# Performance work log

Measured on AMD Instinct MI355X. Metric: run time of the kernel, lower is better.

## Reference

```python
import jax, jax.numpy as jnp
import numpy as np

S, B, D, H, DH = 512, 32, 256, 8, 32  # seq, batch, in_dim, heads, dim_head
LN_EPS = 1e-5


def setup_inputs() -> dict:
    key = jax.random.key(0)
    k1, k2, k3 = jax.random.split(key, 3)
    x = jax.random.normal(k1, (S, B, D), jnp.float32)
    slow_W = jax.random.normal(k2, (H * (5 * DH + 2), D), jnp.float32) * 0.02
    out_W = jax.random.normal(k3, (D, H * DH), jnp.float32) * 0.02
    ln_g = jnp.ones((D,), jnp.float32)
    ln_b = jnp.zeros((D,), jnp.float32)
    return {"x": x, "slow_W": slow_W, "out_W": out_W, "ln_g": ln_g, "ln_b": ln_b}


def elu_p1(x):
    return jax.nn.elu(x) + 1.0


def sum_norm(x):
    return x / jnp.sum(x, axis=-1, keepdims=True)


def layer_norm(x, g, b):
    mu = jnp.mean(x, axis=-1, keepdims=True)
    var = jnp.mean(jnp.square(x - mu), axis=-1, keepdims=True)
    return (x - mu) * jax.lax.rsqrt(var + LN_EPS) * g + b


def _fast_rnn_forward(x, slow_W, out_W, ln_g, ln_b):
    slen, bsz, _ = x.shape
    o = layer_norm(x, ln_g, ln_b)
    qkv = jnp.einsum('sbd,ed->sbe', o, slow_W)  # [S,B,H*(5*DH+2)]
    qkv = qkv.reshape(slen, bsz, H, 5 * DH + 2)
    q, k, v, rk, rv, beta, rbeta = jnp.split(
        qkv, [DH, 2 * DH, 3 * DH, 4 * DH, 5 * DH, 5 * DH + 1], axis=-1)
    beta = jax.nn.sigmoid(beta)      # [S,B,H,1]
    rbeta = jax.nn.sigmoid(rbeta)    # [S,B,H,1]
    q = sum_norm(elu_p1(q))
    k = sum_norm(elu_p1(k))
    rk = jax.nn.softmax(rk, axis=-1)

    # ---- feed-forward fast weights with delta rule (fast_weight_delta) ----
    def ff_step(W, inp):
        qt, kt, vt, bt = inp                      # [B,H,DH], bt [B,H,1]
        v_old = jnp.einsum('bhij,bhj->bhi', W, kt)
        W = W + ((bt * (vt - v_old))[..., :, None] * kt[..., None, :])
        z = jnp.einsum('bhij,bhj->bhi', W, qt)
        return W, z

    W0 = jnp.zeros((bsz, H, DH, DH), x.dtype)
    _, z = jax.lax.scan(ff_step, W0, (q, k, v, beta))  # z: [S,B,H,DH]

    # ---- recurrent fast weights (fast_rnn_v2): query = softmax(prev state) ----
    def rec_step(carry, inp):
        R, h = carry
        zt, kt, vt, bt = inp
        q_rec = jax.nn.softmax(h, axis=-1)         # query from previous state
        v_old = jnp.einsum('bhij,bhj->bhi', R, kt)
        R = R + ((bt * (vt - v_old))[..., :, None] * kt[..., None, :])
        h = zt + jnp.einsum('bhij,bhj->bhi', R, q_rec)
        return (R, h), h

    R0 = jnp.zeros((bsz, H, DH, DH), x.dtype)
    h0 = jnp.zeros((bsz, H, DH), x.dtype)
    _, hs = jax.lax.scan(rec_step, (R0, h0), (z, rk, rv, rbeta))  # [S,B,H,DH]

    out = hs.reshape(slen, bsz, H * DH)
    out = jnp.einsum('sbe,de->sbd', out, out_W)
    return x + out  # dropout is identity in eval


def reference(x, slow_W, out_W, ln_g, ln_b):
    return _fast_rnn_forward(x, slow_W, out_W, ln_g, ln_b)
```

## Files before the change

kernel.cpp:

```cpp
#include <hip/hip_runtime.h>
#include <hip/hip_bf16.h>
#include <math.h>

#define S_   512
#define B_   32
#define D_   256
#define H_   8
#define DH_  32
#define E_   (H_*(5*DH_+2))
#define SB_  (S_*B_)
#define LN_EPSF 1e-5f

#define ROWP_ 164
#define NPAD_ 1344

typedef short  bf16x8 __attribute__((ext_vector_type(8)));
typedef float  f32x4  __attribute__((ext_vector_type(4)));
typedef float  f32x2  __attribute__((ext_vector_type(2)));

__device__ __forceinline__ float wave_sum64(float v){
  #pragma unroll
  for (int m = 32; m >= 1; m >>= 1) v += __shfl_xor(v, m, 64);
  return v;
}
__device__ __forceinline__ float gsum32(float v){
  #pragma unroll
  for (int m = 16; m >= 1; m >>= 1) v += __shfl_xor(v, m, 32);
  return v;
}
__device__ __forceinline__ float gmax32(float v){
  #pragma unroll
  for (int m = 16; m >= 1; m >>= 1) v = fmaxf(v, __shfl_xor(v, m, 32));
  return v;
}

#if __has_builtin(__builtin_amdgcn_permlane32_swap)
typedef int v2i_ __attribute__((ext_vector_type(2)));
__device__ __forceinline__ float xhalf_sum(float x){
  v2i_ r = __builtin_amdgcn_permlane32_swap(__float_as_int(x), __float_as_int(x), false, false);
  return __int_as_float(r.x) + __int_as_float(r.y);
}
#else
__device__ __forceinline__ float xhalf_sum(float x){
  return x + __shfl_xor(x, 32, 64);
}
#endif

#define GL4(dst, sb, vo, IMM) \
  asm volatile("global_load_dwordx4 %0, %1, %2 offset:" IMM \
               : "=&v"(dst) : "v"(vo), "s"(sb))
#define GL2(dst, sb, vo, IMM) \
  asm volatile("global_load_dwordx2 %0, %1, %2 offset:" IMM \
               : "=&v"(dst) : "v"(vo), "s"(sb))
#define GL1(dst, sb, vo, IMM) \
  asm volatile("global_load_dword %0, %1, %2 offset:" IMM \
               : "=&v"(dst) : "v"(vo), "s"(sb))

__global__ __launch_bounds__(256) void ln_kernel(const float* __restrict__ x,
                                                 const float* __restrict__ g,
                                                 const float* __restrict__ b,
                                                 __hip_bfloat16* __restrict__ o){
  __shared__ float sbuf[4];
  const int row = blockIdx.x, tid = threadIdx.x;
  const float v = x[(size_t)row*D_ + tid];
  float s = wave_sum64(v);
  if ((tid & 63) == 0) sbuf[tid >> 6] = s;
  __syncthreads();
  const float mu = (sbuf[0]+sbuf[1]+sbuf[2]+sbuf[3]) * (1.f/D_);
  __syncthreads();
  const float d = v - mu;
  float s2 = wave_sum64(d*d);
  if ((tid & 63) == 0) sbuf[tid >> 6] = s2;
  __syncthreads();
  const float var = (sbuf[0]+sbuf[1]+sbuf[2]+sbuf[3]) * (1.f/D_);
  const float rstd = rsqrtf(var + LN_EPSF);
  o[(size_t)row*D_ + tid] = __float2bfloat16(d*rstd*g[tid] + b[tid]);
}

__global__ __launch_bounds__(256) void cvt_w(const float* __restrict__ W1,
                                             const float* __restrict__ W2,
                                             __hip_bfloat16* __restrict__ o1,
                                             __hip_bfloat16* __restrict__ o2){
  const int r = blockIdx.x, c = threadIdx.x;
  if (r < NPAD_){
    const float v = (r < E_) ? W1[(size_t)r*D_ + c] : 0.f;
    o1[(size_t)r*D_ + c] = __float2bfloat16(v);
  } else {
    const int r2 = r - NPAD_;
    o2[(size_t)r2*D_ + c] = __float2bfloat16(W2[(size_t)r2*D_ + c]);
  }
}

__global__ __launch_bounds__(256) void gemm1_mfma(const __hip_bfloat16* __restrict__ A,
                                                  const __hip_bfloat16* __restrict__ Bw,
                                                  float* __restrict__ qkvT){
  const int tid = threadIdx.x;
  const int w = tid >> 6, l = tid & 63;
  const int lr = l & 15, lk = (l >> 4) << 3;
  const int m0 = blockIdx.y*64 + (w>>1)*32;
  const int n0 = blockIdx.x*64 + (w&1)*32;

  const __hip_bfloat16* Ap = A  + (size_t)(m0+lr)*D_ + lk;
  const __hip_bfloat16* Bp = Bw + (size_t)(n0+lr)*D_ + lk;

  f32x4 acc00={0,0,0,0}, acc01={0,0,0,0}, acc10={0,0,0,0}, acc11={0,0,0,0};
  #pragma unroll
  for (int ks = 0; ks < 8; ++ks){
    const bf16x8 a0 = *(const bf16x8*)(Ap + ks*32);
    const bf16x8 a1 = *(const bf16x8*)(Ap + 16*D_ + ks*32);
    const bf16x8 b0 = *(const bf16x8*)(Bp + ks*32);
    const bf16x8 b1 = *(const bf16x8*)(Bp + 16*D_ + ks*32);
    acc00 = __builtin_amdgcn_mfma_f32_16x16x32_bf16(a0, b0, acc00, 0,0,0);
    acc01 = __builtin_amdgcn_mfma_f32_16x16x32_bf16(a0, b1, acc01, 0,0,0);
    acc10 = __builtin_amdgcn_mfma_f32_16x16x32_bf16(a1, b0, acc10, 0,0,0);
    acc11 = __builtin_amdgcn_mfma_f32_16x16x32_bf16(a1, b1, acc11, 0,0,0);
  }

  const int mrow = (l>>4)<<2;
  #pragma unroll
  for (int i=0;i<2;i++){
    #pragma unroll
    for (int j=0;j<2;j++){
      const f32x4 av = (i==0) ? (j==0?acc00:acc01) : (j==0?acc10:acc11);
      const int n = n0 + j*16 + lr;
      if (n < E_){
        const unsigned head = (unsigned)n / 162u;
        const unsigned jj   = (unsigned)n - head*162u;
        #pragma unroll
        for (int reg=0;reg<4;reg++){
          const int m = m0 + i*16 + mrow + reg;
          const int s = m >> 5, bq = m & 31;
          qkvT[((size_t)(bq*8u+head)*S_ + s)*ROWP_ + jj] = av[reg];
        }
      }
    }
  }
}

__global__ __launch_bounds__(256) void gemm2_mfma(const __hip_bfloat16* __restrict__ A,
                                                  const __hip_bfloat16* __restrict__ Bw,
                                                  const float* __restrict__ X,
                                                  float* __restrict__ C){
  const int tid = threadIdx.x;
  const int w = tid >> 6, l = tid & 63;
  const int lr = l & 15, lk = (l >> 4) << 3;
  const int m0 = blockIdx.y*64 + (w>>1)*32;
  const int n0 = blockIdx.x*64 + (w&1)*32;

  const __hip_bfloat16* Ap = A  + (size_t)(m0+lr)*D_ + lk;
  const __hip_bfloat16* Bp = Bw + (size_t)(n0+lr)*D_ + lk;

  f32x4 acc00={0,0,0,0}, acc01={0,0,0,0}, acc10={0,0,0,0}, acc11={0,0,0,0};
  #pragma unroll
  for (int ks = 0; ks < 8; ++ks){
    const bf16x8 a0 = *(const bf16x8*)(Ap + ks*32);
    const bf16x8 a1 = *(const bf16x8*)(Ap + 16*D_ + ks*32);
    const bf16x8 b0 = *(const bf16x8*)(Bp + ks*32);
    const bf16x8 b1 = *(const bf16x8*)(Bp + 16*D_ + ks*32);
    acc00 = __builtin_amdgcn_mfma_f32_16x16x32_bf16(a0, b0, acc00, 0,0,0);
    acc01 = __builtin_amdgcn_mfma_f32_16x16x32_bf16(a0, b1, acc01, 0,0,0);
    acc10 = __builtin_amdgcn_mfma_f32_16x16x32_bf16(a1, b0, acc10, 0,0,0);
    acc11 = __builtin_amdgcn_mfma_f32_16x16x32_bf16(a1, b1, acc11, 0,0,0);
  }

  const int mrow = (l>>4)<<2;
  #pragma unroll
  for (int i=0;i<2;i++){
    #pragma unroll
    for (int j=0;j<2;j++){
      const f32x4 av = (i==0) ? (j==0?acc00:acc01) : (j==0?acc10:acc11);
      const int n = n0 + j*16 + lr;
      #pragma unroll
      for (int reg=0;reg<4;reg++){
        const size_t m = (size_t)(m0 + i*16 + mrow + reg);
        C[m*D_ + n] = av[reg] + X[m*D_ + n];
      }
    }
  }
}

__global__ __launch_bounds__(256) void act2_kernel(float* __restrict__ qkvT){
  const int row = blockIdx.x*8 + (threadIdx.x >> 5);
  const int i = threadIdx.x & 31;
  float* base = qkvT + (size_t)row*ROWP_;
  float qv  = base[i];
  float kv  = base[DH_ + i];
  float rkv = base[3*DH_ + i];
  qv = qv > 0.f ? qv + 1.f : __expf(qv);
  kv = kv > 0.f ? kv + 1.f : __expf(kv);
  const float qs = gsum32(qv);
  const float ks = gsum32(kv);
  const float rm = gmax32(rkv);
  const float re = __expf(rkv - rm);
  const float rs = gsum32(re);
  base[i]         = qv / qs;
  base[DH_ + i]   = kv / ks;
  base[3*DH_ + i] = re / rs;
  if (i < 2){
    const float bv = base[5*DH_ + i];
    base[5*DH_ + i] = 1.f/(1.f + __expf(-bv));
  }
}

#define SCAN_ISSUE(P, sbp)                                                    \
  { const float* sb_ = (sbp);                                                 \
    GL4(P##q0,  sb_, voP, "0");   GL4(P##q1,  sb_, voP, "16");                \
    GL4(P##q2,  sb_, voP, "32");  GL4(P##q3,  sb_, voP, "48");                \
    GL4(P##k0,  sb_, voP, "128"); GL4(P##k1,  sb_, voP, "144");               \
    GL4(P##k2,  sb_, voP, "160"); GL4(P##k3,  sb_, voP, "176");               \
    GL4(P##rk0, sb_, voP, "384"); GL4(P##rk1, sb_, voP, "400");               \
    GL4(P##rk2, sb_, voP, "416"); GL4(P##rk3, sb_, voP, "432");               \
    GL1(P##v,   sb_, voR, "256"); GL1(P##rv,  sb_, voR, "512");               \
    GL2(P##bb,  sb_, voZ, "640"); }

#define SCAN_BODY(P, tt)                                                      \
  {                                                                           \
             \
    const float e_ = __expf(h);                                               \
    ebuf[r] = e_;                                                             \
    f32x4 ev0 = *(const f32x4*)&ebuf[p16+0];                                  \
    f32x4 ev1 = *(const f32x4*)&ebuf[p16+4];                                  \
    f32x4 ev2 = *(const f32x4*)&ebuf[p16+8];                                  \
    f32x4 ev3 = *(const f32x4*)&ebuf[p16+12];                                 \
                                    \
    if ((tt) >= S_-2) { asm volatile("s_waitcnt vmcnt(0)" ::: "memory"); }    \
    else              { asm volatile("s_waitcnt vmcnt(16)" ::: "memory"); }   \
    __builtin_amdgcn_sched_barrier(0);                                        \
    float q_[16], k_[16], rk_[16];                                            \
    *(f32x4*)&q_[0]=P##q0;  *(f32x4*)&q_[4]=P##q1;                            \
    *(f32x4*)&q_[8]=P##q2;  *(f32x4*)&q_[12]=P##q3;                           \
    *(f32x4*)&k_[0]=P##k0;  *(f32x4*)&k_[4]=P##k1;                            \
    *(f32x4*)&k_[8]=P##k2;  *(f32x4*)&k_[12]=P##k3;                           \
    *(f32x4*)&rk_[0]=P##rk0; *(f32x4*)&rk_[4]=P##rk1;                         \
    *(f32x4*)&rk_[8]=P##rk2; *(f32x4*)&rk_[12]=P##rk3;                        \
    const float vv = P##v, rvv = P##rv;                                       \
    const float beta = P##bb.x, rbeta = P##bb.y;                              \
                                                      \
    float a0=0.f,a1=0.f,a2=0.f,a3=0.f;                                        \
    _Pragma("unroll")                                                         \
    for (int c4=0;c4<16;c4+=4){                                               \
      a0=fmaf(W[c4+0],k_[c4+0],a0); a1=fmaf(W[c4+1],k_[c4+1],a1);             \
      a2=fmaf(W[c4+2],k_[c4+2],a2); a3=fmaf(W[c4+3],k_[c4+3],a3);             \
    }                                                                         \
    const float dot1f = xhalf_sum((a0+a1)+(a2+a3));                           \
    const float coeff = beta*(vv - dot1f);                                    \
    float b0=0.f,b1=0.f,b2=0.f,b3=0.f;                                        \
    _Pragma("unroll")                                                         \
    for (int c4=0;c4<16;c4+=4){                                               \
      W[c4+0]=fmaf(coeff,k_[c4+0],W[c4+0]); b0=fmaf(W[c4+0],q_[c4+0],b0);     \
      W[c4+1]=fmaf(coeff,k_[c4+1],W[c4+1]); b1=fmaf(W[c4+1],q_[c4+1],b1);     \
      W[c4+2]=fmaf(coeff,k_[c4+2],W[c4+2]); b2=fmaf(W[c4+2],q_[c4+2],b2);     \
      W[c4+3]=fmaf(coeff,k_[c4+3],W[c4+3]); b3=fmaf(W[c4+3],q_[c4+3],b3);     \
    }                                                                         \
    const float z_ = xhalf_sum((b0+b1)+(b2+b3));                              \
                            \
    float c0=0.f,c1=0.f,c2=0.f,c3=0.f;                                        \
    _Pragma("unroll")                                                         \
    for (int c4=0;c4<16;c4+=4){                                               \
      c0=fmaf(R[c4+0],rk_[c4+0],c0); c1=fmaf(R[c4+1],rk_[c4+1],c1);           \
      c2=fmaf(R[c4+2],rk_[c4+2],c2); c3=fmaf(R[c4+3],rk_[c4+3],c3);           \
    }                                                                         \
    const float dot1r = xhalf_sum((c0+c1)+(c2+c3));                           \
    const float coefr = rbeta*(rvv - dot1r);                                  \
    _Pragma("unroll")                                                         \
    for (int c4=0;c4<16;c4+=4){                                               \
      R[c4+0]=fmaf(coefr,rk_[c4+0],R[c4+0]); R[c4+1]=fmaf(coefr,rk_[c4+1],R[c4+1]); \
      R[c4+2]=fmaf(coefr,rk_[c4+2],R[c4+2]); R[c4+3]=fmaf(coefr,rk_[c4+3],R[c4+3]); \
    }                                                                         \
      \
    float evv[16];                                                            \
    *(f32x4*)&evv[0]=ev0; *(f32x4*)&evv[4]=ev1;                               \
    *(f32x4*)&evv[8]=ev2; *(f32x4*)&evv[12]=ev3;                              \
    float t0=(evv[0]+evv[1])+(evv[2]+evv[3]),   t1=(evv[4]+evv[5])+(evv[6]+evv[7]); \
    float t2=(evv[8]+evv[9])+(evv[10]+evv[11]), t3=(evv[12]+evv[13])+(evv[14]+evv[15]); \
    const float Ss = xhalf_sum((t0+t1)+(t2+t3));                              \
    float d0=0.f,d1=0.f,d2=0.f,d3=0.f;                                        \
    _Pragma("unroll")                                                         \
    for (int c4=0;c4<16;c4+=4){                                               \
      d0=fmaf(R[c4+0],evv[c4+0],d0); d1=fmaf(R[c4+1],evv[c4+1],d1);           \
      d2=fmaf(R[c4+2],evv[c4+2],d2); d3=fmaf(R[c4+3],evv[c4+3],d3);           \
    }                                                                         \
    const float dot2 = xhalf_sum((d0+d1)+(d2+d3));                            \
    h = fmaf(dot2, __builtin_amdgcn_rcpf(Ss), z_);                            \
    hsb[(size_t)(tt)*(B_*D_) + hoff] = __float2bfloat16(h);                   \
                                       \
    if ((tt)+2 < S_) SCAN_ISSUE(P, gbase + (size_t)((tt)+2)*ROWP_);           \
  }

__global__ __launch_bounds__(64,1) void scan_fused2(const float* __restrict__ qkvT,
                                                    __hip_bfloat16* __restrict__ hsb){
  const int pair = blockIdx.x;
  const int lane = threadIdx.x;
  const int r = lane & 31, p = lane >> 5;
  const int p16 = p*16;
  const int b = pair >> 3, hh = pair & 7;
  const float* gbase = qkvT + (size_t)pair*S_*ROWP_;
  const size_t hoff = (size_t)b*D_ + hh*DH_ + r;

  __shared__ __align__(16) float ebuf[DH_];

  const int voP = p*64;
  const int voR = r*4;
  const int voZ = 0;

  float W[16], R[16];
  #pragma unroll
  for (int i=0;i<16;i++){ W[i]=0.f; R[i]=0.f; }
  float h = 0.f;

  f32x4 Aq0,Aq1,Aq2,Aq3, Ak0,Ak1,Ak2,Ak3, Ark0,Ark1,Ark2,Ark3;
  f32x2 Abb; float Av, Arv;
  f32x4 Bq0,Bq1,Bq2,Bq3, Bk0,Bk1,Bk2,Bk3, Brk0,Brk1,Brk2,Brk3;
  f32x2 Bbb; float Bv, Brv;

  SCAN_ISSUE(A, gbase);
  SCAN_ISSUE(B, gbase + ROWP_);
  asm volatile("s_waitcnt vmcnt(15)" ::: "memory");
  __builtin_amdgcn_sched_barrier(0);

  for (int tc = 0; tc < S_; tc += 2){
    SCAN_BODY(A, tc);
    SCAN_BODY(B, tc+1);
  }
}

extern "C" void kernel_launch(void* const* d_in, const int* in_sizes, int n_in,
                              void* d_out, int out_size, void* d_ws, size_t ws_size,
                              hipStream_t stream) {
  const float* x      = (const float*)d_in[0];
  const float* slow_W = (const float*)d_in[1];
  const float* out_W  = (const float*)d_in[2];
  const float* ln_g   = (const float*)d_in[3];
  const float* ln_b   = (const float*)d_in[4];
  float* out = (float*)d_out;

  float* qkvT = (float*)d_ws;
  __hip_bfloat16* obf  = (__hip_bfloat16*)(qkvT + (size_t)B_*H_*S_*ROWP_);
  __hip_bfloat16* hsb  = obf;
  __hip_bfloat16* w1bf = obf + (size_t)SB_*D_;
  __hip_bfloat16* w2bf = w1bf + (size_t)NPAD_*D_;

  cvt_w<<<NPAD_ + D_, 256, 0, stream>>>(slow_W, out_W, w1bf, w2bf);
  ln_kernel<<<SB_, 256, 0, stream>>>(x, ln_g, ln_b, obf);

  dim3 g1(NPAD_/64, SB_/64);
  gemm1_mfma<<<g1, 256, 0, stream>>>(obf, w1bf, qkvT);

  act2_kernel<<<B_*H_*S_/8, 256, 0, stream>>>(qkvT);

  scan_fused2<<<B_*H_, 64, 0, stream>>>(qkvT, hsb);

  dim3 g2(D_/64, SB_/64);
  gemm2_mfma<<<g2, 256, 0, stream>>>(hsb, w2bf, x, out);
}
```

Baseline: 373.4 us.

## Store qkv intermediate in bf16 with compacted interleaved row layout

The GEMM1 output buffer now holds bf16 instead of fp32, packed into 384-byte rows. A new offset map interleaves v with rv and beta with rbeta, so each pair comes in with a single dword load. The activation kernel and the scan prefetch read and unpack bf16, which roughly halves the bytes each scan step loads and cuts the number of outstanding loads. The cost is that q/k/rk/v lose precision before entering the recurrent scan, which may hurt accuracy over 512 steps.

```diff
diff --git a/kernel.cpp b/kernel.cpp
--- a/kernel.cpp
+++ b/kernel.cpp
@@ -11,12 +11,13 @@
 #define SB_  (S_*B_)
 #define LN_EPSF 1e-5f
 
-#define ROWP_ 164
+#define ROWB_ 384
+#define ROWS_ 192
 #define NPAD_ 1344
 
-typedef short  bf16x8 __attribute__((ext_vector_type(8)));
-typedef float  f32x4  __attribute__((ext_vector_type(4)));
-typedef float  f32x2  __attribute__((ext_vector_type(2)));
+typedef short        bf16x8 __attribute__((ext_vector_type(8)));
+typedef float        f32x4  __attribute__((ext_vector_type(4)));
+typedef unsigned int u32x4  __attribute__((ext_vector_type(4)));
 
 __device__ __forceinline__ float wave_sum64(float v){
   #pragma unroll
@@ -46,11 +47,17 @@
 }
 #endif
 
+__device__ __forceinline__ float bfl(unsigned u){ return __int_as_float((int)(u << 16)); }
+__device__ __forceinline__ float bfh(unsigned u){ return __int_as_float((int)(u & 0xffff0000u)); }
+__device__ __forceinline__ unsigned short bfb(float f){
+  __hip_bfloat16 h = __float2bfloat16(f); return *(unsigned short*)&h;
+}
+__device__ __forceinline__ float bf2f(unsigned short u){
+  return __int_as_float(((int)u) << 16);
+}
+
 #define GL4(dst, sb, vo, IMM) \
   asm volatile("global_load_dwordx4 %0, %1, %2 offset:" IMM \
-               : "=&v"(dst) : "v"(vo), "s"(sb))
-#define GL2(dst, sb, vo, IMM) \
-  asm volatile("global_load_dwordx2 %0, %1, %2 offset:" IMM \
                : "=&v"(dst) : "v"(vo), "s"(sb))
 #define GL1(dst, sb, vo, IMM) \
   asm volatile("global_load_dword %0, %1, %2 offset:" IMM \
@@ -91,9 +98,17 @@
   }
 }
 
+__device__ __forceinline__ int cmp_off(int jj){
+  if (jj < 64)  return 2*jj;
+  if (jj < 96)  return 4*jj - 64;
+  if (jj < 128) return 2*jj - 64;
+  if (jj < 160) return 4*jj - 318;
+  return 320 + 2*(jj - 160);
+}
+
 __global__ __launch_bounds__(256) void gemm1_mfma(const __hip_bfloat16* __restrict__ A,
                                                   const __hip_bfloat16* __restrict__ Bw,
-                                                  float* __restrict__ qkvT){
+                                                  unsigned short* __restrict__ qc){
   const int tid = threadIdx.x;
   const int w = tid >> 6, l = tid & 63;
   const int lr = l & 15, lk = (l >> 4) << 3;
@@ -125,12 +140,14 @@
       const int n = n0 + j*16 + lr;
       if (n < E_){
         const unsigned head = (unsigned)n / 162u;
-        const unsigned jj   = (unsigned)n - head*162u;
+        const int jj = n - (int)head*162;
+        const int off = cmp_off(jj);
         #pragma unroll
         for (int reg=0;reg<4;reg++){
           const int m = m0 + i*16 + mrow + reg;
           const int s = m >> 5, bq = m & 31;
-          qkvT[((size_t)(bq*8u+head)*S_ + s)*ROWP_ + jj] = av[reg];
+          char* rowb = (char*)qc + ((size_t)(bq*8u+head)*S_ + s)*ROWB_;
+          *(unsigned short*)(rowb + off) = bfb(av[reg]);
         }
       }
     }
@@ -179,13 +196,13 @@
   }
 }
 
-__global__ __launch_bounds__(256) void act2_kernel(float* __restrict__ qkvT){
+__global__ __launch_bounds__(256) void act4_kernel(unsigned short* __restrict__ qc){
   const int row = blockIdx.x*8 + (threadIdx.x >> 5);
   const int i = threadIdx.x & 31;
-  float* base = qkvT + (size_t)row*ROWP_;
-  float qv  = base[i];
-  float kv  = base[DH_ + i];
-  float rkv = base[3*DH_ + i];
+  unsigned short* base = qc + (size_t)row*ROWS_;
+  float qv  = bf2f(base[i]);
+  float kv  = bf2f(base[32 + i]);
+  float rkv = bf2f(base[64 + i]);
   qv = qv > 0.f ? qv + 1.f : __expf(qv);
   kv = kv > 0.f ? kv + 1.f : __expf(kv);
   const float qs = gsum32(qv);
@@ -193,25 +210,22 @@
   const float rm = gmax32(rkv);
   const float re = __expf(rkv - rm);
   const float rs = gsum32(re);
-  base[i]         = qv / qs;
-  base[DH_ + i]   = kv / ks;
-  base[3*DH_ + i] = re / rs;
+  base[i]      = bfb(qv / qs);
+  base[32 + i] = bfb(kv / ks);
+  base[64 + i] = bfb(re / rs);
   if (i < 2){
-    const float bv = base[5*DH_ + i];
-    base[5*DH_ + i] = 1.f/(1.f + __expf(-bv));
+    const float bv = bf2f(base[160 + i]);
+    base[160 + i] = bfb(1.f/(1.f + __expf(-bv)));
   }
 }
 
 #define SCAN_ISSUE(P, sbp)                                                    \
-  { const float* sb_ = (sbp);                                                 \
-    GL4(P##q0,  sb_, voP, "0");   GL4(P##q1,  sb_, voP, "16");                \
-    GL4(P##q2,  sb_, voP, "32");  GL4(P##q3,  sb_, voP, "48");                \
-    GL4(P##k0,  sb_, voP, "128"); GL4(P##k1,  sb_, voP, "144");               \
-    GL4(P##k2,  sb_, voP, "160"); GL4(P##k3,  sb_, voP, "176");               \
-    GL4(P##rk0, sb_, voP, "384"); GL4(P##rk1, sb_, voP, "400");               \
-    GL4(P##rk2, sb_, voP, "416"); GL4(P##rk3, sb_, voP, "432");               \
-    GL1(P##v,   sb_, voR, "256"); GL1(P##rv,  sb_, voR, "512");               \
-    GL2(P##bb,  sb_, voZ, "640"); }
+  { const char* sb_ = (sbp);                                                  \
+    GL4(P##q0, sb_, voQ, "0");   GL4(P##q1, sb_, voQ, "16");                  \
+    GL4(P##k0, sb_, voQ, "64");  GL4(P##k1, sb_, voQ, "80");                  \
+    GL4(P##r0, sb_, voQ, "128"); GL4(P##r1, sb_, voQ, "144");                 \
+    GL1(P##vr, sb_, voV, "192");                                              \
+    GL1(P##bb, sb_, voZ, "320"); }
 
 #define SCAN_BODY(P, tt)                                                      \
   {                                                                           \
@@ -224,17 +238,24 @@
     f32x4 ev3 = *(const f32x4*)&ebuf[p16+12];                                 \
                                     \
     if ((tt) >= S_-2) { asm volatile("s_waitcnt vmcnt(0)" ::: "memory"); }    \
-    else              { asm volatile("s_waitcnt vmcnt(16)" ::: "memory"); }   \
+    else              { asm volatile("s_waitcnt vmcnt(9)" ::: "memory"); }    \
     __builtin_amdgcn_sched_barrier(0);                                        \
+                                     \
     float q_[16], k_[16], rk_[16];                                            \
-    *(f32x4*)&q_[0]=P##q0;  *(f32x4*)&q_[4]=P##q1;                            \
-    *(f32x4*)&q_[8]=P##q2;  *(f32x4*)&q_[12]=P##q3;                           \
-    *(f32x4*)&k_[0]=P##k0;  *(f32x4*)&k_[4]=P##k1;                            \
-    *(f32x4*)&k_[8]=P##k2;  *(f32x4*)&k_[12]=P##k3;                           \
-    *(f32x4*)&rk_[0]=P##rk0; *(f32x4*)&rk_[4]=P##rk1;                         \
-    *(f32x4*)&rk_[8]=P##rk2; *(f32x4*)&rk_[12]=P##rk3;                        \
-    const float vv = P##v, rvv = P##rv;                                       \
-    const float beta = P##bb.x, rbeta = P##bb.y;                              \
+    q_[0]=bfl(P##q0[0]);  q_[1]=bfh(P##q0[0]);  q_[2]=bfl(P##q0[1]);  q_[3]=bfh(P##q0[1]); \
+    q_[4]=bfl(P##q0[2]);  q_[5]=bfh(P##q0[2]);  q_[6]=bfl(P##q0[3]);  q_[7]=bfh(P##q0[3]); \
+    q_[8]=bfl(P##q1[0]);  q_[9]=bfh(P##q1[0]);  q_[10]=bfl(P##q1[1]); q_[11]=bfh(P##q1[1]);\
+    q_[12]=bfl(P##q1[2]); q_[13]=bfh(P##q1[2]); q_[14]=bfl(P##q1[3]); q_[15]=bfh(P##q1[3]);\
+    k_[0]=bfl(P##k0[0]);  k_[1]=bfh(P##k0[0]);  k_[2]=bfl(P##k0[1]);  k_[3]=bfh(P##k0[1]); \
+    k_[4]=bfl(P##k0[2]);  k_[5]=bfh(P##k0[2]);  k_[6]=bfl(P##k0[3]);  k_[7]=bfh(P##k0[3]); \
+    k_[8]=bfl(P##k1[0]);  k_[9]=bfh(P##k1[0]);  k_[10]=bfl(P##k1[1]); k_[11]=bfh(P##k1[1]);\
+    k_[12]=bfl(P##k1[2]); k_[13]=bfh(P##k1[2]); k_[14]=bfl(P##k1[3]); k_[15]=bfh(P##k1[3]);\
+    rk_[0]=bfl(P##r0[0]);  rk_[1]=bfh(P##r0[0]);  rk_[2]=bfl(P##r0[1]);  rk_[3]=bfh(P##r0[1]); \
+    rk_[4]=bfl(P##r0[2]);  rk_[5]=bfh(P##r0[2]);  rk_[6]=bfl(P##r0[3]);  rk_[7]=bfh(P##r0[3]); \
+    rk_[8]=bfl(P##r1[0]);  rk_[9]=bfh(P##r1[0]);  rk_[10]=bfl(P##r1[1]); rk_[11]=bfh(P##r1[1]);\
+    rk_[12]=bfl(P##r1[2]); rk_[13]=bfh(P##r1[2]); rk_[14]=bfl(P##r1[3]); rk_[15]=bfh(P##r1[3]);\
+    const float vv   = bfl(P##vr), rvv   = bfh(P##vr);                        \
+    const float beta = bfl(P##bb), rbeta = bfh(P##bb);                        \
                                                       \
     float a0=0.f,a1=0.f,a2=0.f,a3=0.f;                                        \
     _Pragma("unroll")                                                         \
@@ -284,23 +305,23 @@
     h = fmaf(dot2, __builtin_amdgcn_rcpf(Ss), z_);                            \
     hsb[(size_t)(tt)*(B_*D_) + hoff] = __float2bfloat16(h);                   \
                                        \
-    if ((tt)+2 < S_) SCAN_ISSUE(P, gbase + (size_t)((tt)+2)*ROWP_);           \
-  }
-
-__global__ __launch_bounds__(64,1) void scan_fused2(const float* __restrict__ qkvT,
+    if ((tt)+2 < S_) SCAN_ISSUE(P, gbase + (size_t)((tt)+2)*ROWB_);           \
+  }
+
+__global__ __launch_bounds__(64,1) void scan_fused2(const unsigned short* __restrict__ qc,
                                                     __hip_bfloat16* __restrict__ hsb){
   const int pair = blockIdx.x;
   const int lane = threadIdx.x;
   const int r = lane & 31, p = lane >> 5;
   const int p16 = p*16;
   const int b = pair >> 3, hh = pair & 7;
-  const float* gbase = qkvT + (size_t)pair*S_*ROWP_;
+  const char* gbase = (const char*)qc + (size_t)pair*S_*ROWB_;
   const size_t hoff = (size_t)b*D_ + hh*DH_ + r;
 
   __shared__ __align__(16) float ebuf[DH_];
 
-  const int voP = p*64;
-  const int voR = r*4;
+  const int voQ = p*32;
+  const int voV = r*4;
   const int voZ = 0;
 
   float W[16], R[16];
@@ -308,14 +329,12 @@
   for (int i=0;i<16;i++){ W[i]=0.f; R[i]=0.f; }
   float h = 0.f;
 
-  f32x4 Aq0,Aq1,Aq2,Aq3, Ak0,Ak1,Ak2,Ak3, Ark0,Ark1,Ark2,Ark3;
-  f32x2 Abb; float Av, Arv;
-  f32x4 Bq0,Bq1,Bq2,Bq3, Bk0,Bk1,Bk2,Bk3, Brk0,Brk1,Brk2,Brk3;
-  f32x2 Bbb; float Bv, Brv;
+  u32x4 Aq0,Aq1, Ak0,Ak1, Ar0,Ar1; unsigned Avr, Abb;
+  u32x4 Bq0,Bq1, Bk0,Bk1, Br0,Br1; unsigned Bvr, Bbb;
 
   SCAN_ISSUE(A, gbase);
-  SCAN_ISSUE(B, gbase + ROWP_);
-  asm volatile("s_waitcnt vmcnt(15)" ::: "memory");
+  SCAN_ISSUE(B, gbase + ROWB_);
+  asm volatile("s_waitcnt vmcnt(8)" ::: "memory");
   __builtin_amdgcn_sched_barrier(0);
 
   for (int tc = 0; tc < S_; tc += 2){
@@ -334,9 +353,9 @@
   const float* ln_b   = (const float*)d_in[4];
   float* out = (float*)d_out;
 
-  float* qkvT = (float*)d_ws;
-  __hip_bfloat16* obf  = (__hip_bfloat16*)(qkvT + (size_t)B_*H_*S_*ROWP_);
-  __hip_bfloat16* hsb  = obf;
+  unsigned short* qc  = (unsigned short*)d_ws;
+  __hip_bfloat16* obf = (__hip_bfloat16*)((char*)d_ws + (size_t)B_*H_*S_*ROWB_);
+  __hip_bfloat16* hsb = obf;
   __hip_bfloat16* w1bf = obf + (size_t)SB_*D_;
   __hip_bfloat16* w2bf = w1bf + (size_t)NPAD_*D_;
 
@@ -344,11 +363,11 @@
   ln_kernel<<<SB_, 256, 0, stream>>>(x, ln_g, ln_b, obf);
 
   dim3 g1(NPAD_/64, SB_/64);
-  gemm1_mfma<<<g1, 256, 0, stream>>>(obf, w1bf, qkvT);
-
-  act2_kernel<<<B_*H_*S_/8, 256, 0, stream>>>(qkvT);
-
-  scan_fused2<<<B_*H_, 64, 0, stream>>>(qkvT, hsb);
+  gemm1_mfma<<<g1, 256, 0, stream>>>(obf, w1bf, qc);
+
+  act4_kernel<<<B_*H_*S_/8, 256, 0, stream>>>(qc);
+
+  scan_fused2<<<B_*H_, 64, 0, stream>>>(qc, hsb);
 
   dim3 g2(D_/64, SB_/64);
   gemm2_mfma<<<g2, 256, 0, stream>>>(hsb, w2bf, x, out);
```

Result: no change. 366.8 us (median of 2 runs) (-1.8%).
